# Optimization experiments

Measured on AMD Instinct MI355X. Metric: run time of the kernel, lower is better.

Reference implementation:

```python
import jax, jax.numpy as jnp
import numpy as np

B, S, DM, H, DF = 2, 2048, 1024, 16, 4096
HD = DM // H
EPS = 1e-6
NEG = -1e9


def setup_inputs() -> dict:
    key = jax.random.key(0)
    ks = jax.random.split(key, 16)
    sc = 1.0 / np.sqrt(DM)
    scf = 1.0 / np.sqrt(DF)
    return {
        "x": jax.random.normal(ks[0], (B, S, DM), jnp.float32),
        "src_mask": jax.random.randint(ks[1], (B, 1, 1, S), 0, 2, jnp.int32),
        "Wq": jax.random.normal(ks[2], (DM, DM), jnp.float32) * sc,
        "bq": jnp.zeros((DM,), jnp.float32),
        "Wk": jax.random.normal(ks[3], (DM, DM), jnp.float32) * sc,
        "bk": jnp.zeros((DM,), jnp.float32),
        "Wv": jax.random.normal(ks[4], (DM, DM), jnp.float32) * sc,
        "bv": jnp.zeros((DM,), jnp.float32),
        "Wo": jax.random.normal(ks[5], (DM, DM), jnp.float32) * sc,
        "bo": jnp.zeros((DM,), jnp.float32),
        "W1": jax.random.normal(ks[6], (DM, DF), jnp.float32) * sc,
        "b1": jnp.zeros((DF,), jnp.float32),
        "W2": jax.random.normal(ks[7], (DF, DM), jnp.float32) * scf,
        "b2": jnp.zeros((DM,), jnp.float32),
        "alpha1": jnp.ones((1,), jnp.float32),
        "beta1": jnp.ones((1,), jnp.float32),
        "alpha2": jnp.ones((1,), jnp.float32),
        "beta2": jnp.ones((1,), jnp.float32),
    }


def layer_norm(x, alpha, beta):
    # torch: mean + unbiased std (ddof=1), scalar alpha/beta, eps added to std
    mean = jnp.mean(x, axis=-1, keepdims=True)
    std = jnp.std(x, axis=-1, keepdims=True, ddof=1)
    return alpha * (x - mean) / (std + EPS) + beta


def mha(x, mask, Wq, bq, Wk, bk, Wv, bv, Wo, bo):
    def split(t):  # [B,S,DM] -> [B,H,S,HD]
        return t.reshape(B, S, H, HD).transpose(0, 2, 1, 3)
    q = split(x @ Wq + bq)
    k = split(x @ Wk + bk)
    v = split(x @ Wv + bv)
    scores = jnp.einsum("bhqd,bhkd->bhqk", q, k) / np.sqrt(HD)
    scores = jnp.where(mask == 0, NEG, scores)
    probs = jax.nn.softmax(scores, axis=-1)  # dropout in eval mode = identity
    out = jnp.einsum("bhqk,bhkd->bhqd", probs, v)
    out = out.transpose(0, 2, 1, 3).reshape(B, S, DM)
    return out @ Wo + bo


def reference(x, src_mask, Wq, bq, Wk, bk, Wv, bv, Wo, bo, W1, b1, W2, b2,
              alpha1, beta1, alpha2, beta2):
    # pre-norm residual: x + attn(norm(x)); dropout disabled (eval)
    n1 = layer_norm(x, alpha1, beta1)
    h = x + mha(n1, src_mask, Wq, bq, Wk, bk, Wv, bv, Wo, bo)
    n2 = layer_norm(h, alpha2, beta2)
    ff = jax.nn.relu(n2 @ W1 + b1) @ W2 + b2
    return h + ff
```

## Files before the change

kernel.cpp:

```cpp
#include <hip/hip_runtime.h>
#include <hip/hip_bf16.h>

#define SEQ   2048
#define BATCH 2
#define DMODEL 1024
#define DFF   4096
#define NHEAD 16
#define HDIM  64
#define NTOK  (BATCH*SEQ)

typedef short s8v __attribute__((ext_vector_type(8)));
typedef float f4v __attribute__((ext_vector_type(4)));

__device__ __forceinline__ float b2f(unsigned short u) {
    union { unsigned int i; float f; } v; v.i = ((unsigned int)u) << 16; return v.f;
}
__device__ __forceinline__ unsigned short f2b(float f) {
    union { unsigned int i; float f; } v; v.f = f;
    unsigned int r = v.i + 0x7FFFu + ((v.i >> 16) & 1u);
    return (unsigned short)(r >> 16);
}
__device__ __forceinline__ ushort2 cvt_pk(float a, float b) {
    __hip_bfloat162 h = __float22bfloat162_rn(float2{ a, b });
    return *(ushort2*)&h;
}

__device__ __forceinline__ f4v mfma_bf16(s8v a, s8v b, f4v c) {
    return __builtin_amdgcn_mfma_f32_16x16x32_bf16(a, b, c, 0, 0, 0);
}

__device__ __forceinline__ void gload_lds16(const void* g, void* l) {
    __builtin_amdgcn_global_load_lds(
        (const __attribute__((address_space(1))) unsigned int*)g,
        (__attribute__((address_space(3))) unsigned int*)l, 16, 0, 0);
}

template<int N> __device__ __forceinline__ void wait_vmcnt() {
    if constexpr (N == 8)      asm volatile("s_waitcnt vmcnt(8)" ::: "memory");
    else if constexpr (N == 6) asm volatile("s_waitcnt vmcnt(6)" ::: "memory");
    else if constexpr (N == 2) asm volatile("s_waitcnt vmcnt(2)" ::: "memory");
    else                       asm volatile("s_waitcnt vmcnt(0)" ::: "memory");
}

__device__ __forceinline__ void tp_tile(const float* __restrict__ src,
                                        unsigned short* __restrict__ dst,
                                        int R, int C, int br, int bc, int t,
                                        unsigned short* tl) {
    for (int i = 0; i < 16; i++) {
        int idx = t + 256 * i;
        int r = idx >> 6, c = idx & 63;
        tl[r * 65 + c] = f2b(src[(size_t)(br * 64 + r) * C + bc * 64 + c]);
    }
    __syncthreads();
    for (int i = 0; i < 16; i++) {
        int idx = t + 256 * i;
        int r2 = idx >> 6, c2 = idx & 63;
        dst[(size_t)(bc * 64 + r2) * R + br * 64 + c2] = tl[c2 * 65 + r2];
    }
}

__global__ __launch_bounds__(256) void prep_weights(const float* __restrict__ Wq,
                                                    const float* __restrict__ Wk,
                                                    const float* __restrict__ Wv,
                                                    const float* __restrict__ Wo,
                                                    const float* __restrict__ W1,
                                                    const float* __restrict__ W2,
                                                    const float* __restrict__ bq,
                                                    const float* __restrict__ bk,
                                                    const float* __restrict__ bv,
                                                    const float* __restrict__ x,
                                                    const float* __restrict__ a1,
                                                    const float* __restrict__ be1,
                                                    unsigned short* __restrict__ Wqkv_t,
                                                    unsigned short* __restrict__ Wo_t,
                                                    unsigned short* __restrict__ W1_t,
                                                    unsigned short* __restrict__ W2_t,
                                                    float* __restrict__ bqkv,
                                                    unsigned short* __restrict__ n1) {
    __shared__ unsigned short tl[64 * 65];
    __shared__ float red[8];
    const int t = threadIdx.x;
    const int bx = blockIdx.x, by = blockIdx.y, z = blockIdx.z;
    if (z < 4) {
        const float* src = (z == 0) ? Wq : (z == 1) ? Wk : (z == 2) ? Wv : Wo;
        unsigned short* dst = (z == 3) ? Wo_t : Wqkv_t + (size_t)z * 1024 * 1024;
        tp_tile(src, dst, 1024, 1024, bx, by, t, tl);
    } else if (z == 4) {
        for (int i = 0; i < 4; i++) {
            tp_tile(W1, W1_t, 1024, 4096, bx, by + 16 * i, t, tl);
            __syncthreads();
        }
    } else if (z == 5) {
        if (bx == 0 && by == 0) {
            for (int i = 0; i < 12; i++) {
                int idx = t + 256 * i;
                if (idx < 1024) bqkv[idx] = bq[idx];
                else if (idx < 2048) bqkv[idx] = bk[idx - 1024];
                else if (idx < 3072) bqkv[idx] = bv[idx - 2048];
            }
        }
        for (int i = 0; i < 4; i++) {
            tp_tile(W2, W2_t, 4096, 1024, bx + 16 * i, by, t, tl);
            __syncthreads();
        }
    } else {
        const int row = (z - 6) * 256 + by * 16 + bx;
        const float* xr = x + (size_t)row * DMODEL;
        float4 u = ((const float4*)xr)[t];
        float v[4] = { u.x, u.y, u.z, u.w };
        float s = v[0] + v[1] + v[2] + v[3];
        float sq = v[0]*v[0] + v[1]*v[1] + v[2]*v[2] + v[3]*v[3];
        for (int off = 32; off; off >>= 1) { s += __shfl_xor(s, off); sq += __shfl_xor(sq, off); }
        int wave = t >> 6, lane = t & 63;
        if (!lane) { red[wave] = s; red[4 + wave] = sq; }
        __syncthreads();
        s = red[0] + red[1] + red[2] + red[3];
        sq = red[4] + red[5] + red[6] + red[7];
        float mean = s * (1.f / DMODEL);
        float var = (sq - (float)DMODEL * mean * mean) * (1.f / (DMODEL - 1));
        var = var < 0.f ? 0.f : var;
        float inv = a1[0] / (sqrtf(var) + 1e-6f);
        float bt = be1[0];
        uint2 ou;
        unsigned short r0 = f2b((v[0] - mean) * inv + bt);
        unsigned short r1 = f2b((v[1] - mean) * inv + bt);
        unsigned short r2 = f2b((v[2] - mean) * inv + bt);
        unsigned short r3 = f2b((v[3] - mean) * inv + bt);
        ou.x = (unsigned int)r0 | ((unsigned int)r1 << 16);
        ou.y = (unsigned int)r2 | ((unsigned int)r3 << 16);
        ((uint2*)(n1 + (size_t)row * DMODEL))[t] = ou;
    }
}

__global__ __launch_bounds__(256) void mask_scan(const int* __restrict__ msk,
                                                 int* __restrict__ idx,
                                                 float* __restrict__ maskc2,
                                                 int* __restrict__ ntiles) {
    const int b = blockIdx.x, t = threadIdx.x;
    const int base = b * SEQ;
    __shared__ int wsum[4];
    int k[8]; int cnt = 0;
    for (int j = 0; j < 8; j++) {
        k[j] = (msk[base + t * 8 + j] != 0) ? 1 : 0;
        cnt += k[j];
    }
    const int lane = t & 63, wv = t >> 6;
    int pre = cnt;
    for (int off = 1; off < 64; off <<= 1) {
        int n = __shfl_up(pre, off);
        if (lane >= off) pre += n;
    }
    if (lane == 63) wsum[wv] = pre;
    __syncthreads();
    const int Nb = wsum[0] + wsum[1] + wsum[2] + wsum[3];
    int woff = 0;
    for (int w = 0; w < wv; w++) woff += wsum[w];
    const int excl = woff + pre - cnt;
    for (int j = 0; j < 8; j++) {
        int g = t * 8 + j;
        idx[base + g] = 0;
        maskc2[base + g] = (g < Nb) ? 0.f : -1e9f;
    }
    __syncthreads();
    int pos = excl;
    for (int j = 0; j < 8; j++) {
        if (k[j]) { idx[base + pos] = t * 8 + j; pos++; }
    }
    if (t == 0) ntiles[b] = (Nb + 63) >> 6;
}

__global__ __launch_bounds__(256) void pack_kv(const unsigned short* __restrict__ Kb,
                                               const unsigned short* __restrict__ Vb,
                                               const int* __restrict__ idx,
                                               const int* __restrict__ ntiles,
                                               unsigned short* __restrict__ Kc,
                                               unsigned short* __restrict__ Vc) {
    __shared__ unsigned short tl[64 * 65];
    const int t = threadIdx.x;
    const int kt = blockIdx.x, h = blockIdx.y, b = blockIdx.z;
    if (kt >= ntiles[b]) return;
    const int* idxb = idx + b * SEQ + kt * 64;
    const unsigned short* srcK = Kb + (size_t)b * SEQ * 1024 + h * HDIM;
    unsigned short* dstK = Kc + ((size_t)((b * NHEAD + h) * 32 + kt)) * 4096;
    for (int i = 0; i < 2; i++) {
        int ci = t + 256 * i;
        int r = ci >> 3, cp = ci & 7;
        int cl = cp ^ (r & 7);
        int row = idxb[r];
        *(uint4*)&dstK[ci * 8] = *(const uint4*)&srcK[(size_t)row * 1024 + cl * 8];
    }
    const unsigned short* srcV = Vb + (size_t)b * SEQ * 1024 + h * HDIM;
    for (int i = 0; i < 16; i++) {
        int idx2 = t + 256 * i;
        int r = idx2 >> 6, c = idx2 & 63;
        int row = idxb[r];
        tl[r * 65 + c] = srcV[(size_t)row * 1024 + c];
    }
    __syncthreads();
    unsigned short* dstV = Vc + ((size_t)((b * NHEAD + h) * 32 + kt)) * 4096;
    for (int i = 0; i < 2; i++) {
        int ci = t + 256 * i;
        int r = ci >> 3, cp = ci & 7;
        int cl = cp ^ (r & 7);
        ushort4 e0, e1;
        e0.x = tl[(cl * 8 + 0) * 65 + r]; e0.y = tl[(cl * 8 + 1) * 65 + r];
        e0.z = tl[(cl * 8 + 2) * 65 + r]; e0.w = tl[(cl * 8 + 3) * 65 + r];
        e1.x = tl[(cl * 8 + 4) * 65 + r]; e1.y = tl[(cl * 8 + 5) * 65 + r];
        e1.z = tl[(cl * 8 + 6) * 65 + r]; e1.w = tl[(cl * 8 + 7) * 65 + r];
        *(ushort4*)&dstV[ci * 8]     = e0;
        *(ushort4*)&dstV[ci * 8 + 4] = e1;
    }
}

__global__ __launch_bounds__(256) void ln_kernel(const float* __restrict__ x,
                                                 const float* __restrict__ al,
                                                 const float* __restrict__ be,
                                                 unsigned short* __restrict__ o) {
    const int row = blockIdx.x;
    const float* xr = x + (size_t)row * DMODEL;
    float4 u = ((const float4*)xr)[threadIdx.x];
    float v[4] = { u.x, u.y, u.z, u.w };
    float s = v[0] + v[1] + v[2] + v[3];
    float sq = v[0]*v[0] + v[1]*v[1] + v[2]*v[2] + v[3]*v[3];
    for (int off = 32; off; off >>= 1) { s += __shfl_xor(s, off); sq += __shfl_xor(sq, off); }
    __shared__ float red[8];
    int wave = threadIdx.x >> 6, lane = threadIdx.x & 63;
    if (!lane) { red[wave] = s; red[4 + wave] = sq; }
    __syncthreads();
    s = red[0] + red[1] + red[2] + red[3];
    sq = red[4] + red[5] + red[6] + red[7];
    float mean = s * (1.f / DMODEL);
    float var = (sq - (float)DMODEL * mean * mean) * (1.f / (DMODEL - 1));
    var = var < 0.f ? 0.f : var;
    float inv = al[0] / (sqrtf(var) + 1e-6f);
    float bt = be[0];
    uint2 ou;
    unsigned short r0 = f2b((v[0] - mean) * inv + bt);
    unsigned short r1 = f2b((v[1] - mean) * inv + bt);
    unsigned short r2 = f2b((v[2] - mean) * inv + bt);
    unsigned short r3 = f2b((v[3] - mean) * inv + bt);
    ou.x = (unsigned int)r0 | ((unsigned int)r1 << 16);
    ou.y = (unsigned int)r2 | ((unsigned int)r3 << 16);
    ((uint2*)(o + (size_t)row * DMODEL))[threadIdx.x] = ou;
}

template<int BROWS>
__device__ __forceinline__ void stage256(const unsigned short* __restrict__ A,
                                         const unsigned short* __restrict__ Bt,
                                         int m0, int n0, int K, int k0,
                                         unsigned short* sA, unsigned short* sB, int t) {
#pragma unroll
    for (int i = 0; i < 4; i++) {
        int ci = i * 512 + t;
        int r = ci >> 3, c = (ci & 7) ^ (r & 7);
        gload_lds16(A + (size_t)(m0 + r) * K + k0 + c * 8, sA + (size_t)ci * 8);
    }
#pragma unroll
    for (int i = 0; i < BROWS / 64; i++) {
        int ci = i * 512 + t;
        int r = ci >> 3, c = (ci & 7) ^ (r & 7);
        gload_lds16(Bt + (size_t)(n0 + r) * K + k0 + c * 8, sB + (size_t)ci * 8);
    }
}

template<int NFC>
__device__ __forceinline__ void comp256(const unsigned short* sA, const unsigned short* sB,
                                        int wm, int wn, int l16, int quad,
                                        f4v acc[8][NFC]) {
#pragma unroll
    for (int s = 0; s < 2; s++) {
        s8v b[NFC];
#pragma unroll
        for (int ni = 0; ni < NFC; ni++) {
            int r = wn * (NFC * 16) + ni * 16 + l16;
            int p = (s * 4 + quad) ^ (r & 7);
            b[ni] = *(const s8v*)&sB[r * 64 + p * 8];
        }
#pragma unroll
        for (int mi = 0; mi < 8; mi++) {
            int r = wm * 128 + mi * 16 + l16;
            int p = (s * 4 + quad) ^ (r & 7);
            s8v a = *(const s8v*)&sA[r * 64 + p * 8];
#pragma unroll
            for (int ni = 0; ni < NFC; ni++)
                acc[mi][ni] = mfma_bf16(a, b[ni], acc[mi][ni]);
        }
    }
}

template<bool RELU, bool RES, typename CT, bool SPLIT3, int BN>
__global__ __launch_bounds__(512, 2) void gemm256(const unsigned short* __restrict__ A,
                                                  const unsigned short* __restrict__ Bt,
                                                  const float* __restrict__ bias,
                                                  const float* __restrict__ res,
                                                  CT* __restrict__ C,
                                                  float* __restrict__ pbuf,
                                                  int M, int N, int K, int KS) {
    constexpr int NFC = BN / 64;
    constexpr int LPT = 4 + BN / 64;
    __shared__ __align__(16) unsigned short smA[2][256 * 64];
    __shared__ __align__(16) unsigned short smB[2][BN * 64];
    const int t = threadIdx.x;
    const int wave = t >> 6, lane = t & 63;
    const int quad = lane >> 4, l16 = lane & 15;
    const int wm = wave >> 2, wn = wave & 3;
    const int m0 = blockIdx.x * 256, n0 = blockIdx.y * BN;
    const int z = blockIdx.z;
    const int kbeg = z * KS;
    const int nt = KS >> 6;

    f4v acc[8][NFC] = {};

    stage256<BN>(A, Bt, m0, n0, K, kbeg,      smA[0], smB[0], t);
    stage256<BN>(A, Bt, m0, n0, K, kbeg + 64, smA[1], smB[1], t);
    wait_vmcnt<LPT>();
    __builtin_amdgcn_s_barrier();

    for (int it = 0; it < nt - 2; ++it) {
        const int cb = it & 1;
        __builtin_amdgcn_s_setprio(1);
        comp256<NFC>(smA[cb], smB[cb], wm, wn, l16, quad, acc);
        __builtin_amdgcn_s_setprio(0);
        asm volatile("s_waitcnt lgkmcnt(0)" ::: "memory");
        __builtin_amdgcn_s_barrier();
        stage256<BN>(A, Bt, m0, n0, K, kbeg + (it + 2) * 64, smA[cb], smB[cb], t);
        wait_vmcnt<LPT>();
        __builtin_amdgcn_s_barrier();
    }
    {
        const int cb = (nt - 2) & 1;
        __builtin_amdgcn_s_setprio(1);
        comp256<NFC>(smA[cb], smB[cb], wm, wn, l16, quad, acc);
        __builtin_amdgcn_s_setprio(0);
        asm volatile("s_waitcnt vmcnt(0)" ::: "memory");
        __builtin_amdgcn_s_barrier();
    }
    {
        const int cb = (nt - 1) & 1;
        __builtin_amdgcn_s_setprio(1);
        comp256<NFC>(smA[cb], smB[cb], wm, wn, l16, quad, acc);
        __builtin_amdgcn_s_setprio(0);
    }

#pragma unroll
    for (int mi = 0; mi < 8; mi++) {
#pragma unroll
        for (int ni = 0; ni < NFC; ni++) {
            const int col = n0 + wn * (NFC * 16) + ni * 16 + l16;
            const int row0 = m0 + wm * 128 + mi * 16 + quad * 4;
            if (z == 0) {
                const float bv = bias[col];
#pragma unroll
                for (int r = 0; r < 4; r++) {
                    float v = acc[mi][ni][r] + bv;
                    if (RELU) v = v > 0.f ? v : 0.f;
                    if (RES) v += res[(size_t)(row0 + r) * N + col];
                    size_t cidx;
                    if constexpr (SPLIT3)
                        cidx = (size_t)(col >> 10) * ((size_t)NTOK * 1024)
                             + (size_t)(row0 + r) * 1024 + (col & 1023);
                    else
                        cidx = (size_t)(row0 + r) * N + col;
                    if constexpr (sizeof(CT) == 2)
                        C[cidx] = f2b(v);
                    else
                        C[cidx] = v;
                }
            } else {
#pragma unroll
                for (int r = 0; r < 4; r++)
                    pbuf[(size_t)(z - 1) * M * N + (size_t)(row0 + r) * N + col]
                        = acc[mi][ni][r];
            }
        }
    }
}

__global__ __launch_bounds__(256) void add_pbuf(float* __restrict__ out,
                                                const float* __restrict__ pbuf) {
    const int i0 = (blockIdx.x * 256 + threadIdx.x) * 8;
    float4 a0 = *(const float4*)&out[i0];
    float4 a1 = *(const float4*)&out[i0 + 4];
    float4 p0 = *(const float4*)&pbuf[i0];
    float4 p1 = *(const float4*)&pbuf[i0 + 4];
    a0.x += p0.x; a0.y += p0.y; a0.z += p0.z; a0.w += p0.w;
    a1.x += p1.x; a1.y += p1.y; a1.z += p1.z; a1.w += p1.w;
    *(float4*)&out[i0]     = a0;
    *(float4*)&out[i0 + 4] = a1;
}

#define EXPC 0.18033688f
__device__ __forceinline__ void attn_tile(const unsigned short* __restrict__ smKb,
                                          const unsigned short* __restrict__ smVb,
                                          const float* __restrict__ smM, int k0,
                                          unsigned short* __restrict__ smPw,
                                          s8v qf0, s8v qf1, int quad, int l16,
                                          float& l_s, f4v* oacc) {
    const int l7 = l16 & 7;
    f4v s[4];
#pragma unroll
    for (int kt4 = 0; kt4 < 4; kt4++) {
        int r = kt4 * 16 + l16;
        s8v kf0 = *(const s8v*)&smKb[r * 64 + ((quad ^ l7) * 8)];
        s8v kf1 = *(const s8v*)&smKb[r * 64 + (((quad + 4) ^ l7) * 8)];
        f4v z = {};
        z = mfma_bf16(kf0, qf0, z);
        z = mfma_bf16(kf1, qf1, z);
        s[kt4] = z;
    }
#pragma unroll
    for (int kt4 = 0; kt4 < 4; kt4++) {
        float4 mf = *(const float4*)&smM[k0 + kt4 * 16 + quad * 4];
        s[kt4][0] = s[kt4][0] * EXPC + mf.x;
        s[kt4][1] = s[kt4][1] * EXPC + mf.y;
        s[kt4][2] = s[kt4][2] * EXPC + mf.z;
        s[kt4][3] = s[kt4][3] * EXPC + mf.w;
    }
#pragma unroll
    for (int kt4 = 0; kt4 < 4; kt4++)
#pragma unroll
        for (int r = 0; r < 4; r++) {
            float p = __builtin_amdgcn_exp2f(s[kt4][r]);
            s[kt4][r] = p;
            l_s += p;
        }
#pragma unroll
    for (int kt4 = 0; kt4 < 4; kt4++) {
        ushort2 p01 = cvt_pk(s[kt4][0], s[kt4][1]);
        ushort2 p23 = cvt_pk(s[kt4][2], s[kt4][3]);
        ushort4 pk;
        pk.x = p01.x; pk.y = p01.y; pk.z = p23.x; pk.w = p23.y;
        int c = kt4 * 2 + (quad >> 1);
        *(ushort4*)&smPw[l16 * 64 + ((c ^ l7) * 8 + (quad & 1) * 4)] = pk;
    }
    s8v pf0 = *(const s8v*)&smPw[l16 * 64 + ((quad ^ l7) * 8)];
    s8v pf1 = *(const s8v*)&smPw[l16 * 64 + (((quad + 4) ^ l7) * 8)];
#pragma unroll
    for (int nt = 0; nt < 4; nt++) {
        int r = nt * 16 + l16;
        s8v v0 = *(const s8v*)&smVb[r * 64 + ((quad ^ l7) * 8)];
        s8v v1 = *(const s8v*)&smVb[r * 64 + (((quad + 4) ^ l7) * 8)];
        oacc[nt] = mfma_bf16(pf0, v0, oacc[nt]);
        oacc[nt] = mfma_bf16(pf1, v1, oacc[nt]);
    }
}

__global__ __launch_bounds__(512) void attn_kernel(const unsigned short* __restrict__ Qb,
                                                   const unsigned short* __restrict__ Kc,
                                                   const unsigned short* __restrict__ Vc,
                                                   const float* __restrict__ maskc2,
                                                   const int* __restrict__ ntiles,
                                                   unsigned short* __restrict__ out) {
    __shared__ __align__(16) unsigned short smK[2][4096];
    __shared__ __align__(16) unsigned short smV[2][4096];
    __shared__ __align__(16) unsigned short smP[8][1024];
    __shared__ __align__(16) float smM[SEQ];

    const int t = threadIdx.x;
    const int wave = t >> 6, lane = t & 63;
    const int quad = lane >> 4, l16 = lane & 15;
    const int qt = blockIdx.x, h = blockIdx.y, b = blockIdx.z;
    const int q0 = qt * 128 + wave * 16;
    const int nt = ntiles[b];
    const unsigned short* Kbh = Kc + ((size_t)(b * NHEAD + h)) * 32 * 4096;
    const unsigned short* Vbh = Vc + ((size_t)(b * NHEAD + h)) * 32 * 4096;
    unsigned short* smPw = &smP[wave][0];

    const unsigned short* Qp = Qb + ((size_t)b * SEQ + q0 + l16) * 1024 + h * HDIM + quad * 8;
    s8v qf0 = *(const s8v*)(Qp);
    s8v qf1 = *(const s8v*)(Qp + 32);

    gload_lds16(maskc2 + (size_t)b * SEQ + t * 4, (float*)smM + t * 4);
    gload_lds16(Kbh + t * 8,        smK[0] + t * 8);
    gload_lds16(Vbh + t * 8,        smV[0] + t * 8);
    gload_lds16(Kbh + 4096 + t * 8, smK[1] + t * 8);
    gload_lds16(Vbh + 4096 + t * 8, smV[1] + t * 8);
    wait_vmcnt<2>();
    __builtin_amdgcn_s_barrier();

    float l_s = 0.f;
    f4v oacc[4] = {};

    for (int it = 0; it < nt; ++it) {
        const int cb = it & 1;
        __builtin_amdgcn_s_setprio(1);
        attn_tile(smK[cb], smV[cb], smM, it * 64, smPw, qf0, qf1, quad, l16, l_s, oacc);
        __builtin_amdgcn_s_setprio(0);
        if (it + 2 < nt) {
            asm volatile("s_waitcnt lgkmcnt(0)" ::: "memory");
            __builtin_amdgcn_s_barrier();
            gload_lds16(Kbh + (size_t)(it + 2) * 4096 + t * 8, smK[cb] + t * 8);
            gload_lds16(Vbh + (size_t)(it + 2) * 4096 + t * 8, smV[cb] + t * 8);
            wait_vmcnt<2>();
            __builtin_amdgcn_s_barrier();
        } else if (it + 1 < nt) {
            asm volatile("s_waitcnt lgkmcnt(0)" ::: "memory");
            __builtin_amdgcn_s_barrier();
            wait_vmcnt<0>();
            __builtin_amdgcn_s_barrier();
        }
    }

    l_s += __shfl_xor(l_s, 16);
    l_s += __shfl_xor(l_s, 32);
    float lrr[4];
    for (int r = 0; r < 4; r++) lrr[r] = __shfl(l_s, quad * 4 + r);
    for (int nt2 = 0; nt2 < 4; nt2++)
        for (int r = 0; r < 4; r++) {
            int row = q0 + quad * 4 + r;
            int col = h * HDIM + nt2 * 16 + l16;
            out[((size_t)b * SEQ + row) * DMODEL + col] = f2b(oacc[nt2][r] / lrr[r]);
        }
}

extern "C" void kernel_launch(void* const* d_in, const int* in_sizes, int n_in,
                              void* d_out, int out_size, void* d_ws, size_t ws_size,
                              hipStream_t stream) {
    const float* x   = (const float*)d_in[0];
    const int*   msk = (const int*)d_in[1];
    const float* Wq  = (const float*)d_in[2];
    const float* bq  = (const float*)d_in[3];
    const float* Wk  = (const float*)d_in[4];
    const float* bk  = (const float*)d_in[5];
    const float* Wv  = (const float*)d_in[6];
    const float* bv  = (const float*)d_in[7];
    const float* Wo  = (const float*)d_in[8];
    const float* bo  = (const float*)d_in[9];
    const float* W1  = (const float*)d_in[10];
    const float* b1  = (const float*)d_in[11];
    const float* W2  = (const float*)d_in[12];
    const float* b2  = (const float*)d_in[13];
    const float* a1  = (const float*)d_in[14];
    const float* be1 = (const float*)d_in[15];
    const float* a2  = (const float*)d_in[16];
    const float* be2 = (const float*)d_in[17];
    float* outf = (float*)d_out;

    char* ws = (char*)d_ws;
    const size_t MB = 1024 * 1024;
    unsigned short* W2_t   = (unsigned short*)(ws);
    unsigned short* W1_t   = (unsigned short*)(ws + 8 * MB);
    float*          Pbuf   = (float*)(ws + 8 * MB);
    unsigned short* Wqkv_t = (unsigned short*)(ws + 16 * MB);
    float*          bqkv   = (float*)(ws + 22 * MB);
    unsigned short* Kc     = (unsigned short*)(ws + 16 * MB);
    unsigned short* n2     = (unsigned short*)(ws + 16 * MB);
    unsigned short* Wo_t   = (unsigned short*)(ws + 24 * MB);
    unsigned short* Qb     = (unsigned short*)(ws + 26 * MB);
    unsigned short* Kb     = (unsigned short*)(ws + 34 * MB);
    unsigned short* Vb     = (unsigned short*)(ws + 42 * MB);
    float*          Pbuf2  = (float*)(ws + 34 * MB);
    unsigned short* ff1    = (unsigned short*)(ws + 26 * MB);
    unsigned short* attnO  = (unsigned short*)(ws + 50 * MB);
    unsigned short* n1     = (unsigned short*)d_out;
    unsigned short* Vc     = (unsigned short*)d_out;
    float*          hbuf   = (float*)d_out;
    float*          maskc2 = (float*)((char*)d_out + 8 * MB);
    int*            idxc   = (int*)((char*)d_out + 8 * MB + 16 * 1024);
    int*            ntl    = (int*)((char*)d_out + 8 * MB + 32 * 1024);

    mask_scan<<<dim3(BATCH), 256, 0, stream>>>(msk, idxc, maskc2, ntl);
    prep_weights<<<dim3(16, 16, 22), 256, 0, stream>>>(
        Wq, Wk, Wv, Wo, W1, W2, bq, bk, bv, x, a1, be1,
        Wqkv_t, Wo_t, W1_t, W2_t, bqkv, n1);

    gemm256<false, false, unsigned short, true, 256><<<dim3(16, 12, 1), 512, 0, stream>>>(
        n1, Wqkv_t, bqkv, nullptr, Qb, nullptr, NTOK, 3072, 1024, 1024);
    pack_kv<<<dim3(32, 16, 2), 256, 0, stream>>>(Kb, Vb, idxc, ntl, Kc, Vc);
    attn_kernel<<<dim3(16, 16, 2), 512, 0, stream>>>(Qb, Kc, Vc, maskc2, ntl, attnO);
    gemm256<false, true, float, false, 128><<<dim3(16, 8, 2), 512, 0, stream>>>(
        attnO, Wo_t, bo, x, hbuf, Pbuf2, NTOK, 1024, 1024, 512);
    add_pbuf<<<dim3(2048), 256, 0, stream>>>(hbuf, Pbuf2);
    ln_kernel<<<NTOK, 256, 0, stream>>>(hbuf, a2, be2, n2);
    gemm256<true, false, unsigned short, false, 256><<<dim3(16, 16, 1), 512, 0, stream>>>(
        n2, W1_t, b1, nullptr, ff1, nullptr, NTOK, DFF, 1024, 1024);
    gemm256<false, true, float, false, 128><<<dim3(16, 8, 2), 512, 0, stream>>>(
        ff1, W2_t, b2, hbuf, outf, Pbuf, NTOK, 1024, 4096, 2048);
    add_pbuf<<<dim3(2048), 256, 0, stream>>>(outf, Pbuf);
}
```

Baseline: 353.1 us.

## Restructure GEMM main loop into 8-phase half-tile staging interleaved with MFMA

Replaces the two-stage double-buffered loop (compute full tile, then stage the next full tile) with an 8-phase schedule. Each K-tile is split into A/B halves, and the global-to-LDS loads for upcoming halves are issued between four MFMA sub-blocks, separated by barriers. The tile-to-warp row mapping changes so that each warp's A and B fragments fall inside separate halves that can be refilled independently. The aim is to overlap memory traffic with MFMA work more finely, at the cost of more barriers and more complex vmcnt accounting.

```diff
diff --git a/kernel.cpp b/kernel.cpp
--- a/kernel.cpp
+++ b/kernel.cpp
@@ -38,6 +38,7 @@
 template<int N> __device__ __forceinline__ void wait_vmcnt() {
     if constexpr (N == 8)      asm volatile("s_waitcnt vmcnt(8)" ::: "memory");
     else if constexpr (N == 6) asm volatile("s_waitcnt vmcnt(6)" ::: "memory");
+    else if constexpr (N == 4) asm volatile("s_waitcnt vmcnt(4)" ::: "memory");
     else if constexpr (N == 2) asm volatile("s_waitcnt vmcnt(2)" ::: "memory");
     else                       asm volatile("s_waitcnt vmcnt(0)" ::: "memory");
 }
@@ -244,46 +245,145 @@
     ((uint2*)(o + (size_t)row * DMODEL))[threadIdx.x] = ou;
 }
 
-template<int BROWS>
-__device__ __forceinline__ void stage256(const unsigned short* __restrict__ A,
+
+template<int SPAN, int NL>
+__device__ __forceinline__ void stage_half(const unsigned short* __restrict__ mat,
+                                           int base, int K, int k0, int q,
+                                           unsigned short* sdst, int t) {
+#pragma unroll
+    for (int i = 0; i < NL; i++) {
+        int ci = i * 512 + t;
+        int rl = ci >> 3;
+        int c  = (ci & 7) ^ (rl & 7);
+        int gr = (rl / SPAN) * (2 * SPAN) + q * SPAN + (rl % SPAN);
+        gload_lds16(mat + (size_t)(base + gr) * K + k0 + c * 8, sdst + (size_t)ci * 8);
+    }
+}
+
+__device__ __forceinline__ const s8v* afrag(const unsigned short* sA, int mi, int s,
+                                            int wm, int l16, int quad) {
+    int q = mi >> 2;
+    int rl = wm * 64 + (mi & 3) * 16 + l16;
+    return (const s8v*)&sA[q * 8192 + rl * 64 + (((s * 4 + quad) ^ (l16 & 7)) * 8)];
+}
+template<int BN>
+__device__ __forceinline__ const s8v* bfrag(const unsigned short* sB, int ni, int s,
+                                            int wn, int l16, int quad) {
+    constexpr int NQB = BN / 128;
+    int q = ni / NQB;
+    int rl = wn * (BN / 8) + (ni % NQB) * 16 + l16;
+    return (const s8v*)&sB[q * (BN * 32) + rl * 64 + (((s * 4 + quad) ^ (l16 & 7)) * 8)];
+}
+
+template<int BN>
+__device__ __forceinline__ void half_8ph(const unsigned short* __restrict__ A,
                                          const unsigned short* __restrict__ Bt,
-                                         int m0, int n0, int K, int k0,
-                                         unsigned short* sA, unsigned short* sB, int t) {
-#pragma unroll
-    for (int i = 0; i < 4; i++) {
-        int ci = i * 512 + t;
-        int r = ci >> 3, c = (ci & 7) ^ (r & 7);
-        gload_lds16(A + (size_t)(m0 + r) * K + k0 + c * 8, sA + (size_t)ci * 8);
-    }
-#pragma unroll
-    for (int i = 0; i < BROWS / 64; i++) {
-        int ci = i * 512 + t;
-        int r = ci >> 3, c = (ci & 7) ^ (r & 7);
-        gload_lds16(Bt + (size_t)(n0 + r) * K + k0 + c * 8, sB + (size_t)ci * 8);
-    }
-}
-
-template<int NFC>
-__device__ __forceinline__ void comp256(const unsigned short* sA, const unsigned short* sB,
-                                        int wm, int wn, int l16, int quad,
-                                        f4v acc[8][NFC]) {
-#pragma unroll
-    for (int s = 0; s < 2; s++) {
-        s8v b[NFC];
+                                         int m0, int n0, int K, int kT1, int kT2, bool doT2,
+                                         const unsigned short* sAr, const unsigned short* sBr,
+                                         unsigned short* sA_this, unsigned short* sB_this,
+                                         unsigned short* sA_oth,
+                                         int wm, int wn, int l16, int quad, int t,
+                                         f4v acc[8][BN / 64]) {
+    constexpr int NFC = BN / 64, NQB = NFC / 2;
+    constexpr int BSPAN = BN / 8, BNL = BN / 128, BHALF = BN * 32;
+    s8v a[4][2], b[NFC][2];
+#pragma unroll
+    for (int m2 = 0; m2 < 4; m2++) {
+        a[m2][0] = *afrag(sAr, m2, 0, wm, l16, quad);
+        a[m2][1] = *afrag(sAr, m2, 1, wm, l16, quad);
+    }
+#pragma unroll
+    for (int nb = 0; nb < NQB; nb++) {
+        b[nb][0] = *bfrag<BN>(sBr, nb, 0, wn, l16, quad);
+        b[nb][1] = *bfrag<BN>(sBr, nb, 1, wn, l16, quad);
+    }
+    stage_half<64, 2>(A, m0, K, kT1, 1, sA_oth + 8192, t);
+    __builtin_amdgcn_s_barrier();
+    asm volatile("s_waitcnt lgkmcnt(0)" ::: "memory");
+    __builtin_amdgcn_s_setprio(1);
+#pragma unroll
+    for (int m2 = 0; m2 < 4; m2++)
+#pragma unroll
+        for (int nb = 0; nb < NQB; nb++) {
+            acc[m2][nb] = mfma_bf16(a[m2][0], b[nb][0], acc[m2][nb]);
+            acc[m2][nb] = mfma_bf16(a[m2][1], b[nb][1], acc[m2][nb]);
+        }
+    __builtin_amdgcn_s_setprio(0);
+    __builtin_amdgcn_s_barrier();
+#pragma unroll
+    for (int nb = 0; nb < NQB; nb++) {
+        b[NQB + nb][0] = *bfrag<BN>(sBr, NQB + nb, 0, wn, l16, quad);
+        b[NQB + nb][1] = *bfrag<BN>(sBr, NQB + nb, 1, wn, l16, quad);
+    }
+    if (doT2) stage_half<64, 2>(A, m0, K, kT2, 0, sA_this, t);
+    __builtin_amdgcn_s_barrier();
+    asm volatile("s_waitcnt lgkmcnt(0)" ::: "memory");
+    __builtin_amdgcn_s_setprio(1);
+#pragma unroll
+    for (int m2 = 0; m2 < 4; m2++)
+#pragma unroll
+        for (int nb = 0; nb < NQB; nb++) {
+            acc[m2][NQB + nb] = mfma_bf16(a[m2][0], b[NQB + nb][0], acc[m2][NQB + nb]);
+            acc[m2][NQB + nb] = mfma_bf16(a[m2][1], b[NQB + nb][1], acc[m2][NQB + nb]);
+        }
+    __builtin_amdgcn_s_setprio(0);
+    __builtin_amdgcn_s_barrier();
+#pragma unroll
+    for (int m2 = 0; m2 < 4; m2++) {
+        a[m2][0] = *afrag(sAr, 4 + m2, 0, wm, l16, quad);
+        a[m2][1] = *afrag(sAr, 4 + m2, 1, wm, l16, quad);
+    }
+    if (doT2) stage_half<BSPAN, BNL>(Bt, n0, K, kT2, 0, sB_this, t);
+    __builtin_amdgcn_s_barrier();
+    asm volatile("s_waitcnt lgkmcnt(0)" ::: "memory");
+    __builtin_amdgcn_s_setprio(1);
+#pragma unroll
+    for (int m2 = 0; m2 < 4; m2++)
+#pragma unroll
+        for (int nb = 0; nb < NQB; nb++) {
+            acc[4 + m2][nb] = mfma_bf16(a[m2][0], b[nb][0], acc[4 + m2][nb]);
+            acc[4 + m2][nb] = mfma_bf16(a[m2][1], b[nb][1], acc[4 + m2][nb]);
+        }
+    __builtin_amdgcn_s_setprio(0);
+    __builtin_amdgcn_s_barrier();
+    if (doT2) {
+        stage_half<BSPAN, BNL>(Bt, n0, K, kT2, 1, sB_this + BHALF, t);
+        if constexpr (BN == 256) wait_vmcnt<6>(); else wait_vmcnt<4>();
+    } else {
+        wait_vmcnt<0>();
+    }
+    __builtin_amdgcn_s_barrier();
+    __builtin_amdgcn_s_setprio(1);
+#pragma unroll
+    for (int m2 = 0; m2 < 4; m2++)
+#pragma unroll
+        for (int nb = 0; nb < NQB; nb++) {
+            acc[4 + m2][NQB + nb] = mfma_bf16(a[m2][0], b[NQB + nb][0], acc[4 + m2][NQB + nb]);
+            acc[4 + m2][NQB + nb] = mfma_bf16(a[m2][1], b[NQB + nb][1], acc[4 + m2][NQB + nb]);
+        }
+    __builtin_amdgcn_s_setprio(0);
+    __builtin_amdgcn_s_barrier();
+}
+
+template<int BN>
+__device__ __forceinline__ void comp_full(const unsigned short* sA, const unsigned short* sB,
+                                          int wm, int wn, int l16, int quad,
+                                          f4v acc[8][BN / 64]) {
+    constexpr int NFC = BN / 64;
+    s8v b[NFC][2];
+#pragma unroll
+    for (int ni = 0; ni < NFC; ni++) {
+        b[ni][0] = *bfrag<BN>(sB, ni, 0, wn, l16, quad);
+        b[ni][1] = *bfrag<BN>(sB, ni, 1, wn, l16, quad);
+    }
+#pragma unroll
+    for (int mi = 0; mi < 8; mi++) {
+        s8v a0 = *afrag(sA, mi, 0, wm, l16, quad);
+        s8v a1 = *afrag(sA, mi, 1, wm, l16, quad);
 #pragma unroll
         for (int ni = 0; ni < NFC; ni++) {
-            int r = wn * (NFC * 16) + ni * 16 + l16;
-            int p = (s * 4 + quad) ^ (r & 7);
-            b[ni] = *(const s8v*)&sB[r * 64 + p * 8];
-        }
-#pragma unroll
-        for (int mi = 0; mi < 8; mi++) {
-            int r = wm * 128 + mi * 16 + l16;
-            int p = (s * 4 + quad) ^ (r & 7);
-            s8v a = *(const s8v*)&sA[r * 64 + p * 8];
-#pragma unroll
-            for (int ni = 0; ni < NFC; ni++)
-                acc[mi][ni] = mfma_bf16(a, b[ni], acc[mi][ni]);
+            acc[mi][ni] = mfma_bf16(a0, b[ni][0], acc[mi][ni]);
+            acc[mi][ni] = mfma_bf16(a1, b[ni][1], acc[mi][ni]);
         }
     }
 }
@@ -297,7 +397,7 @@
                                                   float* __restrict__ pbuf,
                                                   int M, int N, int K, int KS) {
     constexpr int NFC = BN / 64;
-    constexpr int LPT = 4 + BN / 64;
+    constexpr int BHALF = BN * 32;
     __shared__ __align__(16) unsigned short smA[2][256 * 64];
     __shared__ __align__(16) unsigned short smB[2][BN * 64];
     const int t = threadIdx.x;
@@ -311,36 +411,31 @@
 
     f4v acc[8][NFC] = {};
 
-    stage256<BN>(A, Bt, m0, n0, K, kbeg,      smA[0], smB[0], t);
-    stage256<BN>(A, Bt, m0, n0, K, kbeg + 64, smA[1], smB[1], t);
-    wait_vmcnt<LPT>();
-    __builtin_amdgcn_s_barrier();
-
-    for (int it = 0; it < nt - 2; ++it) {
-        const int cb = it & 1;
-        __builtin_amdgcn_s_setprio(1);
-        comp256<NFC>(smA[cb], smB[cb], wm, wn, l16, quad, acc);
-        __builtin_amdgcn_s_setprio(0);
-        asm volatile("s_waitcnt lgkmcnt(0)" ::: "memory");
-        __builtin_amdgcn_s_barrier();
-        stage256<BN>(A, Bt, m0, n0, K, kbeg + (it + 2) * 64, smA[cb], smB[cb], t);
-        wait_vmcnt<LPT>();
-        __builtin_amdgcn_s_barrier();
-    }
-    {
-        const int cb = (nt - 2) & 1;
-        __builtin_amdgcn_s_setprio(1);
-        comp256<NFC>(smA[cb], smB[cb], wm, wn, l16, quad, acc);
-        __builtin_amdgcn_s_setprio(0);
-        asm volatile("s_waitcnt vmcnt(0)" ::: "memory");
-        __builtin_amdgcn_s_barrier();
-    }
-    {
-        const int cb = (nt - 1) & 1;
-        __builtin_amdgcn_s_setprio(1);
-        comp256<NFC>(smA[cb], smB[cb], wm, wn, l16, quad, acc);
-        __builtin_amdgcn_s_setprio(0);
-    }
+    stage_half<64, 2>(A, m0, K, kbeg, 0, smA[0], t);
+    stage_half<64, 2>(A, m0, K, kbeg, 1, smA[0] + 8192, t);
+    stage_half<BN / 8, BN / 128>(Bt, n0, K, kbeg, 0, smB[0], t);
+    stage_half<BN / 8, BN / 128>(Bt, n0, K, kbeg, 1, smB[0] + BHALF, t);
+    stage_half<64, 2>(A, m0, K, kbeg + 64, 0, smA[1], t);
+    stage_half<BN / 8, BN / 128>(Bt, n0, K, kbeg + 64, 0, smB[1], t);
+    stage_half<BN / 8, BN / 128>(Bt, n0, K, kbeg + 64, 1, smB[1] + BHALF, t);
+    if constexpr (BN == 256) wait_vmcnt<6>(); else wait_vmcnt<4>();
+    __builtin_amdgcn_s_barrier();
+
+    for (int i = 0; i < nt / 2 - 1; ++i) {
+        const int kb = kbeg + 2 * i * 64;
+        half_8ph<BN>(A, Bt, m0, n0, K, kb + 64, kb + 128, true,
+                     smA[0], smB[0], smA[0], smB[0], smA[1],
+                     wm, wn, l16, quad, t, acc);
+        half_8ph<BN>(A, Bt, m0, n0, K, kb + 128, kb + 192, true,
+                     smA[1], smB[1], smA[1], smB[1], smA[0],
+                     wm, wn, l16, quad, t, acc);
+    }
+    half_8ph<BN>(A, Bt, m0, n0, K, kbeg + (nt - 1) * 64, 0, false,
+                 smA[0], smB[0], smA[0], smB[0], smA[1],
+                 wm, wn, l16, quad, t, acc);
+    __builtin_amdgcn_s_setprio(1);
+    comp_full<BN>(smA[1], smB[1], wm, wn, l16, quad, acc);
+    __builtin_amdgcn_s_setprio(0);
 
 #pragma unroll
     for (int mi = 0; mi < 8; mi++) {
```

Result: faster. 343.9 us (-2.6%).
